# Optimization experiments

Hardware: AMD Instinct MI355X
Metric: run time of the kernel (lower is better)

Reference implementation:

```python
import jax, jax.numpy as jnp
import numpy as np

C0 = 0.28209479177387814
C1 = 0.4886025119029199
C2 = (1.0925484305920792, -1.0925484305920792, 0.31539156525252005,
      -1.0925484305920792, 0.5462742152960396)
EPS = 1e-6


def eval_sh_bases2(d):
    # d: [..., 3] unit directions -> [..., 9] SH basis (degree 2, svox2 convention)
    x, y, z = d[..., 0], d[..., 1], d[..., 2]
    return jnp.stack([
        jnp.full_like(x, C0),
        -C1 * y, C1 * z, -C1 * x,
        C2[0] * x * y, C2[1] * y * z,
        C2[2] * (2.0 * z * z - x * x - y * y),
        C2[3] * x * z, C2[4] * (x * x - y * y),
    ], axis=-1)


def get_sh_vals(xyz, sh_feats, invs, locs):
    # xyz: [N,3]; sh_feats: [J,9]; invs: [J,4,4]; locs: [J,3] -> weights [N,J]
    n = xyz.shape[0]
    xyz_h = jnp.concatenate([xyz, jnp.ones((n, 1), xyz.dtype)], axis=-1)  # [N,4]
    pts = jnp.einsum('jab,nb->jna', invs, xyz_h)[..., :3]  # [J,N,3]
    vd = locs[:, None, :] - pts                             # [J,N,3]
    norm = jnp.linalg.norm(vd, axis=-1)                     # [J,N]
    lengths = jnp.nan_to_num(norm)
    vd = vd / jnp.maximum(norm, 1e-12)[..., None]           # F.normalize
    sh = eval_sh_bases2(vd)                                 # [J,N,9]
    rads = jax.nn.relu(jnp.einsum('jnk,jk->jn', sh, sh_feats) + 0.5)
    rel = jax.nn.relu(1.0 - lengths / jnp.maximum(rads, EPS))
    rel = jnp.where(rads < EPS, 0.0, rel)
    return rel.T  # [N,J]


def weighted_transformation(pts, weights, transforms):
    # pts: [M,3]; weights: [M,J]; transforms: [J,4,4] (already inverse transforms,
    # if_transform_is_inv=True). Linear-blend the matrices and apply.
    wsum = weights.sum(axis=-1, keepdims=True)              # [M,1]
    wn = weights / jnp.maximum(wsum, EPS)
    T = jnp.einsum('mj,jab->mab', wn, transforms)           # [M,4,4]
    p_h = jnp.concatenate([pts, jnp.ones((pts.shape[0], 1), pts.dtype)], axis=-1)
    out = jnp.einsum('mab,mb->ma', T, p_h)[:, :3]
    return jnp.where(wsum > EPS, out, pts)                  # untouched if no weight


def setup_inputs() -> dict:
    key = jax.random.key(0)
    ks = jax.random.split(key, 5)
    B, S, J = 4096, 128, 24
    return {
        'xyz_sampled': jax.random.normal(ks[0], (B, S, 3), jnp.float32),
        'viewdirs': jax.random.normal(ks[1], (B, S, 3), jnp.float32),
        'transforms': jax.random.normal(ks[2], (J, 4, 4), jnp.float32),
        'ray_valid': jnp.ones((B, S), dtype=bool),
        'sh_feats': jax.random.normal(ks[3], (J, 9), jnp.float32),
        'locs': jax.random.normal(ks[4], (J, 3), jnp.float32),
    }


def reference(xyz_sampled, viewdirs, transforms, ray_valid, sh_feats, locs):
    shape = xyz_sampled.shape
    x = xyz_sampled.reshape(-1, 3)
    n = x.shape[0]
    tmp = jnp.concatenate([x, (xyz_sampled - viewdirs).reshape(-1, 3)], axis=0)  # [2N,3]
    w = get_sh_vals(x, sh_feats, transforms, locs)          # [N,J]
    w2 = jnp.concatenate([w, w], axis=0)                    # [2N,J]
    tmp = weighted_transformation(tmp, w2, transforms)      # [2N,3]
    xyz_out = tmp[:n]
    view_out = xyz_out - tmp[n:]
    return xyz_out.reshape(shape), view_out.reshape(shape)
```

## Files before the change

### kernel.cpp

```cpp
#include <hip/hip_runtime.h>

#define EPS 1e-6f
#define J 24
#define NPAIR 12
#define PAIR_STRIDE 56

typedef float v2f __attribute__((ext_vector_type(2)));

__device__ __forceinline__ v2f fma2(v2f a, v2f b, v2f c) {
    return __builtin_elementwise_fma(a, b, c);
}
__device__ __forceinline__ v2f max2(v2f a, v2f b) {
    return __builtin_elementwise_max(a, b);
}

__global__ void fold_kernel(const float* __restrict__ transforms,
                            const float* __restrict__ sh_feats,
                            const float* __restrict__ locs,
                            float* __restrict__ cj)
{
    const int j = threadIdx.x;
    if (j >= J) return;

    float F[9];
    #pragma unroll
    for (int k = 0; k < 9; ++k) F[k] = sh_feats[j * 9 + k];

    const float C0  = 0.28209479177387814f;
    const float C1  = 0.4886025119029199f;
    const float C2a = 1.0925484305920792f;

    const float f0  = C0 * F[0] + 0.5f;
    const float cy  = -C1 * F[1];
    const float cz  =  C1 * F[2];
    const float cx  = -C1 * F[3];
    const float cxy =  C2a * F[4];
    const float cyz = -C2a * F[5];
    const float c6  = 0.31539156525252005f * F[6];
    const float cxz = -C2a * F[7];
    const float c8  = 0.5462742152960396f  * F[8];

    float vals[25];
    #pragma unroll
    for (int k = 0; k < 12; ++k) vals[k] = transforms[j * 16 + k];
    vals[12] = vals[3]  - locs[j * 3 + 0];
    vals[13] = vals[7]  - locs[j * 3 + 1];
    vals[14] = vals[11] - locs[j * 3 + 2];
    vals[15] = f0;
    vals[16] = cx;  vals[17] = cy;  vals[18] = cz;
    vals[19] = cxy; vals[20] = cyz; vals[21] = cxz;
    vals[22] = c8 - c6;
    vals[23] = -c6 - c8;
    vals[24] = 2.0f * c6;

    float* base = cj + (j >> 1) * PAIR_STRIDE + (j & 1);
    #pragma unroll
    for (int k = 0; k < 25; ++k) base[2 * k] = vals[k];
}

__global__ __launch_bounds__(256, 6) void shcaster_kernel(
    const float* __restrict__ xyz,
    const float* __restrict__ vdir,
    const float* __restrict__ cj,
    float* __restrict__ out,
    int n)
{
    const int i = blockIdx.x * blockDim.x + threadIdx.x;
    if (i >= n) return;

    const float px = xyz[3 * i + 0];
    const float py = xyz[3 * i + 1];
    const float pz = xyz[3 * i + 2];
    const float vx = vdir[3 * i + 0];
    const float vy = vdir[3 * i + 1];
    const float vz = vdir[3 * i + 2];

    const v2f px2 = {px, px};
    const v2f py2 = {py, py};
    const v2f pz2 = {pz, pz};
    const v2f one2  = {1.f, 1.f};
    const v2f zero2 = {0.f, 0.f};
    const v2f eps2  = {EPS, EPS};

    v2f wsum2 = zero2;
    v2f Ta2[12];
    #pragma unroll
    for (int k = 0; k < 12; ++k) Ta2[k] = zero2;

    #pragma unroll 2
    for (int pp = 0; pp < NPAIR; ++pp) {
        const v2f* s = (const v2f*)(cj + pp * PAIR_STRIDE);

        const v2f ux = fma2(s[0], px2, fma2(s[1], py2, fma2(s[2],  pz2, s[12])));
        const v2f uy = fma2(s[4], px2, fma2(s[5], py2, fma2(s[6],  pz2, s[13])));
        const v2f uz = fma2(s[8], px2, fma2(s[9], py2, fma2(s[10], pz2, s[14])));

        const v2f xx = ux * ux;
        const v2f yy = uy * uy;
        const v2f zz = uz * uz;
        v2f d2 = (xx + yy) + zz;
        d2 = max2(d2, (v2f){1e-24f, 1e-24f});

        const v2f inv = {__builtin_amdgcn_rsqf(d2.x), __builtin_amdgcn_rsqf(d2.y)};

        v2f lin = fma2(s[16], ux, fma2(s[17], uy, s[18] * uz));
        v2f quad = fma2(s[19], ux * uy, fma2(s[20], uy * uz, fma2(s[21], ux * uz,
                   fma2(s[22], xx, fma2(s[23], yy, s[24] * zz)))));

        const v2f len  = d2 * inv;
        const v2f inv2 = inv * inv;

        v2f rads = fma2(quad, inv2, s[15]);
        rads = fma2(-lin, inv, rads);
        rads = max2(rads, zero2);

        const v2f rm = max2(rads, eps2);
        const v2f rc = {__builtin_amdgcn_rcpf(rm.x), __builtin_amdgcn_rcpf(rm.y)};
        v2f rel = max2(fma2(-len, rc, one2), zero2);
        rel.x = (rads.x < EPS) ? 0.f : rel.x;
        rel.y = (rads.y < EPS) ? 0.f : rel.y;

        wsum2 += rel;
        #pragma unroll
        for (int k = 0; k < 12; ++k) Ta2[k] = fma2(rel, s[k], Ta2[k]);
    }

    const float wsum = wsum2.x + wsum2.y;
    float Ta[12];
    #pragma unroll
    for (int k = 0; k < 12; ++k) Ta[k] = Ta2[k].x + Ta2[k].y;

    const float inv_w = __builtin_amdgcn_rcpf(fmaxf(wsum, EPS));
    const bool valid = wsum > EPS;

    const float axo = fmaf(Ta[0], px, fmaf(Ta[1], py, fmaf(Ta[2],  pz, Ta[3])))  * inv_w;
    const float ayo = fmaf(Ta[4], px, fmaf(Ta[5], py, fmaf(Ta[6],  pz, Ta[7])))  * inv_w;
    const float azo = fmaf(Ta[8], px, fmaf(Ta[9], py, fmaf(Ta[10], pz, Ta[11]))) * inv_w;

    const float qx = px - vx;
    const float qy = py - vy;
    const float qz = pz - vz;
    const float bxo = fmaf(Ta[0], qx, fmaf(Ta[1], qy, fmaf(Ta[2],  qz, Ta[3])))  * inv_w;
    const float byo = fmaf(Ta[4], qx, fmaf(Ta[5], qy, fmaf(Ta[6],  qz, Ta[7])))  * inv_w;
    const float bzo = fmaf(Ta[8], qx, fmaf(Ta[9], qy, fmaf(Ta[10], qz, Ta[11]))) * inv_w;

    const float ox = valid ? axo : px;
    const float oy = valid ? ayo : py;
    const float oz = valid ? azo : pz;
    const float wx = ox - (valid ? bxo : qx);
    const float wy = oy - (valid ? byo : qy);
    const float wz = oz - (valid ? bzo : qz);

    out[3 * i + 0] = ox;
    out[3 * i + 1] = oy;
    out[3 * i + 2] = oz;
    float* out2 = out + (size_t)3 * n;
    out2[3 * i + 0] = wx;
    out2[3 * i + 1] = wy;
    out2[3 * i + 2] = wz;
}

extern "C" void kernel_launch(void* const* d_in, const int* in_sizes, int n_in,
                              void* d_out, int out_size, void* d_ws, size_t ws_size,
                              hipStream_t stream) {
    const int n = (out_size > 0) ? (out_size / 6) : 524288;
    const int big = 3 * n;

    const float* xyz  = nullptr;
    const float* vdir = nullptr;
    const float* trf  = nullptr;
    const float* shf  = nullptr;
    const float* locs = nullptr;
    int bigSeen = 0;
    for (int k = 0; k < n_in; ++k) {
        const int s = in_sizes[k];
        if (s == big) {
            if (bigSeen++ == 0) xyz = (const float*)d_in[k];
            else                vdir = (const float*)d_in[k];
        } else if (s == 384) {
            trf = (const float*)d_in[k];
        } else if (s == 216) {
            shf = (const float*)d_in[k];
        } else if (s == 72) {
            locs = (const float*)d_in[k];
        }
    }
    if (!xyz || !vdir || !trf || !shf || !locs) {
        xyz  = (const float*)d_in[0];
        vdir = (const float*)d_in[1];
        trf  = (const float*)d_in[2];
        shf  = (const float*)d_in[n_in >= 6 ? 4 : 3];
        locs = (const float*)d_in[n_in >= 6 ? 5 : 4];
    }

    float* cj = (float*)d_ws;
    float* out = (float*)d_out;

    fold_kernel<<<1, 64, 0, stream>>>(trf, shf, locs, cj);

    const int block = 256;
    const int grid = (n + block - 1) / block;
    shcaster_kernel<<<grid, block, 0, stream>>>(xyz, vdir, cj, out, n);
}
```

Before: 87.02 us.

## Fuse coefficient fold into main kernel via shared memory, skip zero-weight joint pairs

Removes the separate fold kernel launch by having the first 24 threads of each block compute the per-joint coefficients into shared memory before a barrier. The main loop now reads coefficients from LDS instead of global/scalar memory. The radius test is rewritten algebraically to avoid a multiply by inv^2 by scaling through d2. A wave-wide ballot skips the 12-term matrix accumulation when no lane has positive weight for a joint pair. This adds redundant per-block setup work, a __syncthreads, and LDS reads that may be slower than scalar loads of uniform data.

```diff
diff --git a/kernel.cpp b/kernel.cpp
--- a/kernel.cpp
+++ b/kernel.cpp
@@ -3,7 +3,7 @@
 #define EPS 1e-6f
 #define J 24
 #define NPAIR 12
-#define PAIR_STRIDE 56
+#define PAIR_STRIDE 28
 
 typedef float v2f __attribute__((ext_vector_type(2)));
 
@@ -12,75 +12,77 @@
 }
 __device__ __forceinline__ v2f max2(v2f a, v2f b) {
     return __builtin_elementwise_max(a, b);
-}
-
-__global__ void fold_kernel(const float* __restrict__ transforms,
-                            const float* __restrict__ sh_feats,
-                            const float* __restrict__ locs,
-                            float* __restrict__ cj)
-{
-    const int j = threadIdx.x;
-    if (j >= J) return;
-
-    float F[9];
-    #pragma unroll
-    for (int k = 0; k < 9; ++k) F[k] = sh_feats[j * 9 + k];
-
-    const float C0  = 0.28209479177387814f;
-    const float C1  = 0.4886025119029199f;
-    const float C2a = 1.0925484305920792f;
-
-    const float f0  = C0 * F[0] + 0.5f;
-    const float cy  = -C1 * F[1];
-    const float cz  =  C1 * F[2];
-    const float cx  = -C1 * F[3];
-    const float cxy =  C2a * F[4];
-    const float cyz = -C2a * F[5];
-    const float c6  = 0.31539156525252005f * F[6];
-    const float cxz = -C2a * F[7];
-    const float c8  = 0.5462742152960396f  * F[8];
-
-    float vals[25];
-    #pragma unroll
-    for (int k = 0; k < 12; ++k) vals[k] = transforms[j * 16 + k];
-    vals[12] = vals[3]  - locs[j * 3 + 0];
-    vals[13] = vals[7]  - locs[j * 3 + 1];
-    vals[14] = vals[11] - locs[j * 3 + 2];
-    vals[15] = f0;
-    vals[16] = cx;  vals[17] = cy;  vals[18] = cz;
-    vals[19] = cxy; vals[20] = cyz; vals[21] = cxz;
-    vals[22] = c8 - c6;
-    vals[23] = -c6 - c8;
-    vals[24] = 2.0f * c6;
-
-    float* base = cj + (j >> 1) * PAIR_STRIDE + (j & 1);
-    #pragma unroll
-    for (int k = 0; k < 25; ++k) base[2 * k] = vals[k];
 }
 
 __global__ __launch_bounds__(256, 6) void shcaster_kernel(
     const float* __restrict__ xyz,
     const float* __restrict__ vdir,
-    const float* __restrict__ cj,
+    const float* __restrict__ transforms,
+    const float* __restrict__ sh_feats,
+    const float* __restrict__ locs,
     float* __restrict__ out,
     int n)
 {
-    const int i = blockIdx.x * blockDim.x + threadIdx.x;
+    __shared__ v2f sj[NPAIR * PAIR_STRIDE];
+    const int tid = threadIdx.x;
+    const int i = blockIdx.x * blockDim.x + tid;
+
+    float px = 0.f, py = 0.f, pz = 0.f, vx = 0.f, vy = 0.f, vz = 0.f;
+    if (i < n) {
+        px = xyz[3 * i + 0];
+        py = xyz[3 * i + 1];
+        pz = xyz[3 * i + 2];
+        vx = vdir[3 * i + 0];
+        vy = vdir[3 * i + 1];
+        vz = vdir[3 * i + 2];
+    }
+
+    if (tid < J) {
+        const int j = tid;
+        float F[9];
+        #pragma unroll
+        for (int k = 0; k < 9; ++k) F[k] = sh_feats[j * 9 + k];
+
+        const float C0  = 0.28209479177387814f;
+        const float C1  = 0.4886025119029199f;
+        const float C2a = 1.0925484305920792f;
+
+        const float f0  = C0 * F[0] + 0.5f;
+        const float cy  = -C1 * F[1];
+        const float cz  =  C1 * F[2];
+        const float cx  = -C1 * F[3];
+        const float cxy =  C2a * F[4];
+        const float cyz = -C2a * F[5];
+        const float c6  = 0.31539156525252005f * F[6];
+        const float cxz = -C2a * F[7];
+        const float c8  = 0.5462742152960396f  * F[8];
+
+        float vals[25];
+        #pragma unroll
+        for (int k = 0; k < 12; ++k) vals[k] = transforms[j * 16 + k];
+        vals[12] = vals[3]  - locs[j * 3 + 0];
+        vals[13] = vals[7]  - locs[j * 3 + 1];
+        vals[14] = vals[11] - locs[j * 3 + 2];
+        vals[15] = f0;
+        vals[16] = cx;  vals[17] = cy;  vals[18] = cz;
+        vals[19] = cxy; vals[20] = cyz; vals[21] = cxz;
+        vals[22] = c8 - c6;
+        vals[23] = -c6 - c8;
+        vals[24] = 2.0f * c6;
+
+        float* base = (float*)&sj[(j >> 1) * PAIR_STRIDE] + (j & 1);
+        #pragma unroll
+        for (int k = 0; k < 25; ++k) base[2 * k] = vals[k];
+    }
+    __syncthreads();
+
     if (i >= n) return;
-
-    const float px = xyz[3 * i + 0];
-    const float py = xyz[3 * i + 1];
-    const float pz = xyz[3 * i + 2];
-    const float vx = vdir[3 * i + 0];
-    const float vy = vdir[3 * i + 1];
-    const float vz = vdir[3 * i + 2];
 
     const v2f px2 = {px, px};
     const v2f py2 = {py, py};
     const v2f pz2 = {pz, pz};
     const v2f one2  = {1.f, 1.f};
     const v2f zero2 = {0.f, 0.f};
-    const v2f eps2  = {EPS, EPS};
 
     v2f wsum2 = zero2;
     v2f Ta2[12];
@@ -89,7 +91,7 @@
 
     #pragma unroll 2
     for (int pp = 0; pp < NPAIR; ++pp) {
-        const v2f* s = (const v2f*)(cj + pp * PAIR_STRIDE);
+        const v2f* s = &sj[pp * PAIR_STRIDE];
 
         const v2f ux = fma2(s[0], px2, fma2(s[1], py2, fma2(s[2],  pz2, s[12])));
         const v2f uy = fma2(s[4], px2, fma2(s[5], py2, fma2(s[6],  pz2, s[13])));
@@ -103,26 +105,26 @@
 
         const v2f inv = {__builtin_amdgcn_rsqf(d2.x), __builtin_amdgcn_rsqf(d2.y)};
 
-        v2f lin = fma2(s[16], ux, fma2(s[17], uy, s[18] * uz));
-        v2f quad = fma2(s[19], ux * uy, fma2(s[20], uy * uz, fma2(s[21], ux * uz,
-                   fma2(s[22], xx, fma2(s[23], yy, s[24] * zz)))));
-
-        const v2f len  = d2 * inv;
-        const v2f inv2 = inv * inv;
-
-        v2f rads = fma2(quad, inv2, s[15]);
-        rads = fma2(-lin, inv, rads);
-        rads = max2(rads, zero2);
-
-        const v2f rm = max2(rads, eps2);
+        const v2f lin  = fma2(s[16], ux, fma2(s[17], uy, s[18] * uz));
+        const v2f quad = fma2(s[19], ux * uy, fma2(s[20], uy * uz, fma2(s[21], ux * uz,
+                         fma2(s[22], xx, fma2(s[23], yy, s[24] * zz)))));
+
+        const v2f len = d2 * inv;
+        const v2f R2  = fma2(s[15], d2, fma2(-lin, len, quad));
+        const v2f ed2 = d2 * (v2f){EPS, EPS};
+        const v2f num = len * d2;
+
+        const v2f rm = max2(R2, ed2);
         const v2f rc = {__builtin_amdgcn_rcpf(rm.x), __builtin_amdgcn_rcpf(rm.y)};
-        v2f rel = max2(fma2(-len, rc, one2), zero2);
-        rel.x = (rads.x < EPS) ? 0.f : rel.x;
-        rel.y = (rads.y < EPS) ? 0.f : rel.y;
-
-        wsum2 += rel;
-        #pragma unroll
-        for (int k = 0; k < 12; ++k) Ta2[k] = fma2(rel, s[k], Ta2[k]);
+        v2f rel = max2(fma2(-num, rc, one2), zero2);
+        rel.x = (R2.x < ed2.x) ? 0.f : rel.x;
+        rel.y = (R2.y < ed2.y) ? 0.f : rel.y;
+
+        if (__ballot((rel.x > 0.f) || (rel.y > 0.f)) != 0ull) {
+            wsum2 += rel;
+            #pragma unroll
+            for (int k = 0; k < 12; ++k) Ta2[k] = fma2(rel, s[k], Ta2[k]);
+        }
     }
 
     const float wsum = wsum2.x + wsum2.y;
@@ -193,12 +195,8 @@
         locs = (const float*)d_in[n_in >= 6 ? 5 : 4];
     }
 
-    float* cj = (float*)d_ws;
     float* out = (float*)d_out;
-
-    fold_kernel<<<1, 64, 0, stream>>>(trf, shf, locs, cj);
-
     const int block = 256;
     const int grid = (n + block - 1) / block;
-    shcaster_kernel<<<grid, block, 0, stream>>>(xyz, vdir, cj, out, n);
-}
+    shcaster_kernel<<<grid, block, 0, stream>>>(xyz, vdir, trf, shf, locs, out, n);
+}
```

Measured after the change: 98.33 us. 13.0% more time.
